# Performance work log

Measured on AMD Instinct MI355X. Metric: run time of the kernel, lower is better.

## Reference

```python
import jax, jax.numpy as jnp
import numpy as np

B, S, H = 2, 2048, 2048
E, I, SH = 8, 768, 5632
TOP_K = 2


def setup_inputs() -> dict:
    key = jax.random.key(0)
    ks = jax.random.split(key, 8)
    sc = lambda *shape: 1.0 / np.sqrt(shape[-2] if len(shape) > 1 else 1.0)
    return {
        "hidden_states": jax.random.normal(ks[0], (B, S, H), jnp.float32),
        "router_w": jax.random.normal(ks[1], (H, E), jnp.float32) * (1.0 / np.sqrt(H)),
        "expert_gate_up_w": jax.random.normal(ks[2], (E, H, 2 * I), jnp.float32) * (1.0 / np.sqrt(H)),
        "expert_down_w": jax.random.normal(ks[3], (E, I, H), jnp.float32) * (1.0 / np.sqrt(I)),
        "shared_gate_w": jax.random.normal(ks[4], (H, SH), jnp.float32) * (1.0 / np.sqrt(H)),
        "shared_up_w": jax.random.normal(ks[5], (H, SH), jnp.float32) * (1.0 / np.sqrt(H)),
        "shared_down_w": jax.random.normal(ks[6], (SH, H), jnp.float32) * (1.0 / np.sqrt(SH)),
        "shared_expert_gate_w": jax.random.normal(ks[7], (H, 1), jnp.float32) * (1.0 / np.sqrt(H)),
    }


def reference(hidden_states, router_w, expert_gate_up_w, expert_down_w,
              shared_gate_w, shared_up_w, shared_down_w, shared_expert_gate_w):
    b, s, h = hidden_states.shape
    x = hidden_states.reshape(-1, h)  # [T, H]

    # Shared expert (SwiGLU) gated by sigmoid scalar gate per token.
    gate = jax.nn.silu((x @ shared_gate_w).astype(jnp.float32)).astype(x.dtype)
    shared_out = (gate * (x @ shared_up_w)) @ shared_down_w  # [T, H]
    shared_out = jax.nn.sigmoid(x @ shared_expert_gate_w) * shared_out

    # Router: softmax -> top-k -> renormalize -> dense routing weights [E, T].
    router_logits = x @ router_w  # [T, E]
    router_probs = jax.nn.softmax(router_logits, axis=-1)
    top_p, top_i = jax.lax.top_k(router_probs, TOP_K)  # [T, k]
    top_p = top_p / jnp.sum(top_p, axis=-1, keepdims=True)
    one_hot = jax.nn.one_hot(top_i, E, dtype=top_p.dtype)  # [T, k, E]
    routing_full = jnp.sum(one_hot * top_p[..., None], axis=1)  # [T, E]
    routing_full = routing_full.T.astype(x.dtype)  # [E, T]

    # Dense per-expert SwiGLU over all tokens (as in source einsums).
    gate_up = jnp.einsum('th,ehm->etm', x, expert_gate_up_w)  # [E, T, 2I]
    g, u = jnp.split(gate_up, 2, axis=-1)
    g = jax.nn.silu(g.astype(jnp.float32)).astype(x.dtype)
    expert_out = jnp.einsum('eti,eih->eth', u * g, expert_down_w)  # [E, T, H]

    expert_contribution = jnp.sum(expert_out * routing_full[:, :, None], axis=0)  # [T, H]
    out = (expert_contribution + shared_out).reshape(b, s, h)
    return out, router_logits
```

## Files before the change

### kernel.cpp

```cpp
#include <hip/hip_runtime.h>
#include <hip/hip_bf16.h>
#include <stdint.h>

#define DEVFN static __device__ __forceinline__

typedef __attribute__((ext_vector_type(8))) short bf16x8;
typedef __attribute__((ext_vector_type(4))) float f32x4;
typedef unsigned short u16;
typedef unsigned int u32;
typedef unsigned long long u64;

DEVFN u16 f2bf(float f) {
    union { float f; u32 u; } v; v.f = f;
    u32 r = v.u + 0x7FFFu + ((v.u >> 16) & 1u);
    return (u16)(r >> 16);
}

DEVFN void g2l16(const void* g, void* l) {
    __builtin_amdgcn_global_load_lds(
        (const __attribute__((address_space(1))) u32*)g,
        (__attribute__((address_space(3))) u32*)l, 16, 0, 0);
}

DEVFN void hbar() {
    __asm__ __volatile__("" ::: "memory");
    __builtin_amdgcn_s_barrier();
    __asm__ __volatile__("" ::: "memory");
}
DEVFN void vm4() { asm volatile("s_waitcnt vmcnt(4)" ::: "memory"); }
DEVFN void vm0() { asm volatile("s_waitcnt vmcnt(0)" ::: "memory"); }

#define MFMA16(a, b, c) __builtin_amdgcn_mfma_f32_16x16x32_bf16(a, b, c, 0, 0, 0)

__global__ __launch_bounds__(512, 2) void gemm8_swiglu_k(
    const u16* __restrict__ A, const u16* __restrict__ Bg,
    const u16* __restrict__ Bu, u16* __restrict__ out,
    int K, int nx, int ldc)
{
    extern __shared__ char smraw[];
    char* smA = smraw;
    char* smB = smraw + 65536;

    const int tid = threadIdx.x;
    const int lane = tid & 63, wv = tid >> 6;
    const int wm = wv >> 2, wn = wv & 3;
    const int l15 = lane & 15, kg = lane >> 4;

    const int nwg = gridDim.x;
    const int id = (blockIdx.x & 7) * (nwg >> 3) + (blockIdx.x >> 3);
    const int m0 = (id / nx) * 256, n0 = (id % nx) * 128;

    const u16* Ap  = A  + (long)m0 * K;
    const u16* Bgp = Bg + (long)n0 * K;
    const u16* Bup = Bu + (long)n0 * K;

    f32x4 accg[8][2], accu[8][2];
#pragma unroll
    for (int i = 0; i < 8; ++i)
#pragma unroll
        for (int j = 0; j < 2; ++j) {
            accg[i][j] = f32x4{0.f, 0.f, 0.f, 0.f};
            accu[i][j] = f32x4{0.f, 0.f, 0.f, 0.f};
        }

    auto stA = [&](int kt, int hh, int buf) {
        const u16* src = Ap + ((long)hh * 128) * K + kt * 64;
        char* dst = smA + buf * 32768 + hh * 16384;
#pragma unroll
        for (int i = 0; i < 2; ++i) {
            int slot = i * 512 + tid;
            int row = slot >> 3, ch = slot & 7;
            g2l16(src + (long)row * K + ((ch ^ (row & 7)) << 3), dst + slot * 16);
        }
    };
    auto stB = [&](int kt, int hh, int buf) {
        const u16* src = (hh ? Bup : Bgp) + kt * 64;
        char* dst = smB + buf * 32768 + hh * 16384;
#pragma unroll
        for (int i = 0; i < 2; ++i) {
            int slot = i * 512 + tid;
            int row = slot >> 3, ch = slot & 7;
            g2l16(src + (long)row * K + ((ch ^ (row & 7)) << 3), dst + slot * 16);
        }
    };
    auto frag = [&](const char* base, int r, int c) -> bf16x8 {
        return *(const __attribute__((address_space(3))) bf16x8*)
            (base + r * 128 + (((c) ^ (r & 7)) << 4));
    };

    stA(0, 0, 0); stA(0, 1, 0);
    stB(0, 0, 0); stB(0, 1, 0);
    stB(1, 0, 1); stB(1, 1, 1);
    vm4();
    hbar();

    const int nk = K >> 6;
    for (int kt = 0; kt < nk; kt += 2) {
        const bool more = (kt + 2) < nk;
#pragma unroll
        for (int h = 0; h < 2; ++h) {
            const char* ab = smA + h * 32768;
            const char* bb = smB + h * 32768;
            bf16x8 bgv[2][2], buv[2][2];
#pragma unroll
            for (int p = 0; p < 4; ++p) {
                if (p == 0) {
#pragma unroll
                    for (int fn = 0; fn < 2; ++fn)
#pragma unroll
                        for (int s = 0; s < 2; ++s) {
                            int rB = wn * 32 + fn * 16 + l15;
                            bgv[fn][s] = frag(bb, rB, s * 4 + kg);
                            buv[fn][s] = frag(bb + 16384, rB, s * 4 + kg);
                        }
                }
                bf16x8 av[2][2];
#pragma unroll
                for (int am = 0; am < 2; ++am)
#pragma unroll
                    for (int s = 0; s < 2; ++s)
                        av[am][s] = frag(ab, wm * 128 + (p * 2 + am) * 16 + l15,
                                         s * 4 + kg);
                if (h == 0) {
                    if (p == 0)      { stA(kt + 1, 0, 1); stA(kt + 1, 1, 1); }
                    else if (p == 1) { if (more) stB(kt + 2, 0, 0); }
                    else if (p == 2) { if (more) stB(kt + 2, 1, 0); }
                    else             { if (more) vm4(); else vm0(); }
                } else {
                    if (more) {
                        if (p == 0)      stA(kt + 2, 0, 0);
                        else if (p == 1) stA(kt + 2, 1, 0);
                        else if (p == 2) stB(kt + 3, 0, 1);
                        else             { stB(kt + 3, 1, 1); vm4(); }
                    }
                }
                hbar();
                __builtin_amdgcn_sched_barrier(0);
                __builtin_amdgcn_s_setprio(1);
#pragma unroll
                for (int am = 0; am < 2; ++am)
#pragma unroll
                    for (int s = 0; s < 2; ++s)
#pragma unroll
                        for (int fn = 0; fn < 2; ++fn) {
                            accg[p * 2 + am][fn] = MFMA16(av[am][s], bgv[fn][s],
                                                          accg[p * 2 + am][fn]);
                            accu[p * 2 + am][fn] = MFMA16(av[am][s], buv[fn][s],
                                                          accu[p * 2 + am][fn]);
                        }
                __builtin_amdgcn_s_setprio(0);
                __builtin_amdgcn_sched_barrier(0);
                hbar();
            }
        }
    }

    const int lq = lane >> 4;
#pragma unroll
    for (int fm = 0; fm < 8; ++fm)
#pragma unroll
        for (int j = 0; j < 4; ++j) {
            int row = m0 + wm * 128 + fm * 16 + lq * 4 + j;
#pragma unroll
            for (int fn = 0; fn < 2; ++fn) {
                int col = n0 + wn * 32 + fn * 16 + l15;
                float g = accg[fm][fn][j], u = accu[fm][fn][j];
                float s = g * (1.f / (1.f + __expf(-g))) * u;
                out[(long)row * ldc + col] = f2bf(s);
            }
        }
}

__global__ __launch_bounds__(512, 2) void gemm8e_swiglu_k(
    const u16* __restrict__ xb, const u16* __restrict__ Beg,
    const u16* __restrict__ Beu, const int* __restrict__ tok,
    const int* __restrict__ cntp, u16* __restrict__ eact,
    int K, int ldc, int cap)
{
    const int e = blockIdx.z;
    const int m0 = blockIdx.y * 256;
    if (m0 >= cntp[e]) return;
    const int n0 = blockIdx.x * 128;

    extern __shared__ char smraw[];
    char* smA = smraw;
    char* smB = smraw + 65536;

    const int tid = threadIdx.x;
    const int lane = tid & 63, wv = tid >> 6;
    const int wm = wv >> 2, wn = wv & 3;
    const int l15 = lane & 15, kg = lane >> 4;

    const int r0 = tid >> 3, ch = tid & 7;
    const int swz = (ch ^ (r0 & 7)) << 3;
    const int* tseg = tok + (long)e * cap + m0;
    const u16* pa00 = xb + (long)tseg[r0] * K + swz;
    const u16* pa01 = xb + (long)tseg[64 + r0] * K + swz;
    const u16* pa10 = xb + (long)tseg[128 + r0] * K + swz;
    const u16* pa11 = xb + (long)tseg[192 + r0] * K + swz;

    const u16* Bgp = Beg + ((long)e * ldc + n0) * K;
    const u16* Bup = Beu + ((long)e * ldc + n0) * K;

    f32x4 accg[8][2], accu[8][2];
#pragma unroll
    for (int i = 0; i < 8; ++i)
#pragma unroll
        for (int j = 0; j < 2; ++j) {
            accg[i][j] = f32x4{0.f, 0.f, 0.f, 0.f};
            accu[i][j] = f32x4{0.f, 0.f, 0.f, 0.f};
        }

    auto stA = [&](int kt, int hh, int buf) {
        char* dst = smA + buf * 32768 + hh * 16384;
        const u16* p0 = hh ? pa10 : pa00;
        const u16* p1 = hh ? pa11 : pa01;
        g2l16(p0 + kt * 64, dst + (long)tid * 16);
        g2l16(p1 + kt * 64, dst + (long)(512 + tid) * 16);
    };
    auto stB = [&](int kt, int hh, int buf) {
        const u16* src = (hh ? Bup : Bgp) + kt * 64;
        char* dst = smB + buf * 32768 + hh * 16384;
#pragma unroll
        for (int i = 0; i < 2; ++i) {
            int slot = i * 512 + tid;
            int row = slot >> 3, c = slot & 7;
            g2l16(src + (long)row * K + ((c ^ (row & 7)) << 3), dst + slot * 16);
        }
    };
    auto frag = [&](const char* base, int r, int c) -> bf16x8 {
        return *(const __attribute__((address_space(3))) bf16x8*)
            (base + r * 128 + (((c) ^ (r & 7)) << 4));
    };

    stA(0, 0, 0); stA(0, 1, 0);
    stB(0, 0, 0); stB(0, 1, 0);
    stB(1, 0, 1); stB(1, 1, 1);
    vm4();
    hbar();

    const int nk = K >> 6;
    for (int kt = 0; kt < nk; kt += 2) {
        const bool more = (kt + 2) < nk;
#pragma unroll
        for (int h = 0; h < 2; ++h) {
            const char* ab = smA + h * 32768;
            const char* bb = smB + h * 32768;
            bf16x8 bgv[2][2], buv[2][2];
#pragma unroll
            for (int p = 0; p < 4; ++p) {
                if (p == 0) {
#pragma unroll
                    for (int fn = 0; fn < 2; ++fn)
#pragma unroll
                        for (int s = 0; s < 2; ++s) {
                            int rB = wn * 32 + fn * 16 + l15;
                            bgv[fn][s] = frag(bb, rB, s * 4 + kg);
                            buv[fn][s] = frag(bb + 16384, rB, s * 4 + kg);
                        }
                }
                bf16x8 av[2][2];
#pragma unroll
                for (int am = 0; am < 2; ++am)
#pragma unroll
                    for (int s = 0; s < 2; ++s)
                        av[am][s] = frag(ab, wm * 128 + (p * 2 + am) * 16 + l15,
                                         s * 4 + kg);
                if (h == 0) {
                    if (p == 0)      { stA(kt + 1, 0, 1); stA(kt + 1, 1, 1); }
                    else if (p == 1) { if (more) stB(kt + 2, 0, 0); }
                    else if (p == 2) { if (more) stB(kt + 2, 1, 0); }
                    else             { if (more) vm4(); else vm0(); }
                } else {
                    if (more) {
                        if (p == 0)      stA(kt + 2, 0, 0);
                        else if (p == 1) stA(kt + 2, 1, 0);
                        else if (p == 2) stB(kt + 3, 0, 1);
                        else             { stB(kt + 3, 1, 1); vm4(); }
                    }
                }
                hbar();
                __builtin_amdgcn_sched_barrier(0);
                __builtin_amdgcn_s_setprio(1);
#pragma unroll
                for (int am = 0; am < 2; ++am)
#pragma unroll
                    for (int s = 0; s < 2; ++s)
#pragma unroll
                        for (int fn = 0; fn < 2; ++fn) {
                            accg[p * 2 + am][fn] = MFMA16(av[am][s], bgv[fn][s],
                                                          accg[p * 2 + am][fn]);
                            accu[p * 2 + am][fn] = MFMA16(av[am][s], buv[fn][s],
                                                          accu[p * 2 + am][fn]);
                        }
                __builtin_amdgcn_s_setprio(0);
                __builtin_amdgcn_sched_barrier(0);
                hbar();
            }
        }
    }

    const int lq = lane >> 4;
#pragma unroll
    for (int fm = 0; fm < 8; ++fm)
#pragma unroll
        for (int j = 0; j < 4; ++j) {
            long row = (long)e * cap + m0 + wm * 128 + fm * 16 + lq * 4 + j;
#pragma unroll
            for (int fn = 0; fn < 2; ++fn) {
                int col = n0 + wn * 32 + fn * 16 + l15;
                float g = accg[fm][fn][j], u = accu[fm][fn][j];
                float s = g * (1.f / (1.f + __expf(-g))) * u;
                eact[row * ldc + col] = f2bf(s);
            }
        }
}

__global__ __launch_bounds__(512, 2) void gemm8_downks_k(
    const u16* __restrict__ A, const u16* __restrict__ B,
    float* __restrict__ out, const float* __restrict__ sig,
    int K, int nkh, int ldc)
{
    extern __shared__ char smraw[];
    char* smA = smraw;
    char* smB = smraw + 65536;

    const int tid = threadIdx.x;
    const int lane = tid & 63, wv = tid >> 6;
    const int wm = wv >> 2, wn = wv & 3;
    const int l15 = lane & 15, kg = lane >> 4;

    const int m0 = blockIdx.y * 256, n0 = blockIdx.x * 256;
    const long k0 = (long)blockIdx.z * nkh * 64;

    const u16* Ap  = A + (long)m0 * K + k0;
    const u16* Blo = B + (long)n0 * K + k0;
    const u16* Bhi = B + (long)(n0 + 128) * K + k0;

    f32x4 accg[8][2], accu[8][2];
#pragma unroll
    for (int i = 0; i < 8; ++i)
#pragma unroll
        for (int j = 0; j < 2; ++j) {
            accg[i][j] = f32x4{0.f, 0.f, 0.f, 0.f};
            accu[i][j] = f32x4{0.f, 0.f, 0.f, 0.f};
        }

    auto stA = [&](int kt, int hh, int buf) {
        const u16* src = Ap + ((long)hh * 128) * K + kt * 64;
        char* dst = smA + buf * 32768 + hh * 16384;
#pragma unroll
        for (int i = 0; i < 2; ++i) {
            int slot = i * 512 + tid;
            int row = slot >> 3, ch = slot & 7;
            g2l16(src + (long)row * K + ((ch ^ (row & 7)) << 3), dst + slot * 16);
        }
    };
    auto stB = [&](int kt, int hh, int buf) {
        const u16* src = (hh ? Bhi : Blo) + kt * 64;
        char* dst = smB + buf * 32768 + hh * 16384;
#pragma unroll
        for (int i = 0; i < 2; ++i) {
            int slot = i * 512 + tid;
            int row = slot >> 3, ch = slot & 7;
            g2l16(src + (long)row * K + ((ch ^ (row & 7)) << 3), dst + slot * 16);
        }
    };
    auto frag = [&](const char* base, int r, int c) -> bf16x8 {
        return *(const __attribute__((address_space(3))) bf16x8*)
            (base + r * 128 + (((c) ^ (r & 7)) << 4));
    };

    stA(0, 0, 0); stA(0, 1, 0);
    stB(0, 0, 0); stB(0, 1, 0);
    stB(1, 0, 1); stB(1, 1, 1);
    vm4();
    hbar();

    const int nk = nkh;
    for (int kt = 0; kt < nk; kt += 2) {
        const bool more = (kt + 2) < nk;
#pragma unroll
        for (int h = 0; h < 2; ++h) {
            const char* ab = smA + h * 32768;
            const char* bb = smB + h * 32768;
            bf16x8 bgv[2][2], buv[2][2];
#pragma unroll
            for (int p = 0; p < 4; ++p) {
                if (p == 0) {
#pragma unroll
                    for (int fn = 0; fn < 2; ++fn)
#pragma unroll
                        for (int s = 0; s < 2; ++s) {
                            int rB = wn * 32 + fn * 16 + l15;
                            bgv[fn][s] = frag(bb, rB, s * 4 + kg);
                            buv[fn][s] = frag(bb + 16384, rB, s * 4 + kg);
                        }
                }
                bf16x8 av[2][2];
#pragma unroll
                for (int am = 0; am < 2; ++am)
#pragma unroll
                    for (int s = 0; s < 2; ++s)
                        av[am][s] = frag(ab, wm * 128 + (p * 2 + am) * 16 + l15,
                                         s * 4 + kg);
                if (h == 0) {
                    if (p == 0)      { stA(kt + 1, 0, 1); stA(kt + 1, 1, 1); }
                    else if (p == 1) { if (more) stB(kt + 2, 0, 0); }
                    else if (p == 2) { if (more) stB(kt + 2, 1, 0); }
                    else             { if (more) vm4(); else vm0(); }
                } else {
                    if (more) {
                        if (p == 0)      stA(kt + 2, 0, 0);
                        else if (p == 1) stA(kt + 2, 1, 0);
                        else if (p == 2) stB(kt + 3, 0, 1);
                        else             { stB(kt + 3, 1, 1); vm4(); }
                    }
                }
                hbar();
                __builtin_amdgcn_sched_barrier(0);
                __builtin_amdgcn_s_setprio(1);
#pragma unroll
                for (int am = 0; am < 2; ++am)
#pragma unroll
                    for (int s = 0; s < 2; ++s)
#pragma unroll
                        for (int fn = 0; fn < 2; ++fn) {
                            accg[p * 2 + am][fn] = MFMA16(av[am][s], bgv[fn][s],
                                                          accg[p * 2 + am][fn]);
                            accu[p * 2 + am][fn] = MFMA16(av[am][s], buv[fn][s],
                                                          accu[p * 2 + am][fn]);
                        }
                __builtin_amdgcn_s_setprio(0);
                __builtin_amdgcn_sched_barrier(0);
                hbar();
            }
        }
    }

    const int lq = lane >> 4;
#pragma unroll
    for (int fm = 0; fm < 8; ++fm)
#pragma unroll
        for (int j = 0; j < 4; ++j) {
            int row = m0 + wm * 128 + fm * 16 + lq * 4 + j;
            float s = sig[row];
#pragma unroll
            for (int fn = 0; fn < 2; ++fn) {
                int col = n0 + wn * 32 + fn * 16 + l15;
                atomicAdd(out + (long)row * ldc + col, accg[fm][fn][j] * s);
                atomicAdd(out + (long)row * ldc + col + 128, accu[fm][fn][j] * s);
            }
        }
}

template<int NSLOT>
DEVFN void stage(const u16* __restrict__ src, int ldk, u16* lds, int tid) {
#pragma unroll
    for (int i = 0; i < NSLOT / 256; ++i) {
        int slot = i * 256 + tid;
        int row = slot >> 2, chunk = slot & 3;
        int kg = chunk ^ ((row >> 1) & 3);
        g2l16(src + (long)row * ldk + kg * 8, lds + slot * 8);
    }
}

DEVFN bf16x8 ld_frag(const u16* lds, int row, int kg) {
    int chunk = kg ^ ((row >> 1) & 3);
    const u16* p = lds + row * 32 + chunk * 8;
    return *(const __attribute__((address_space(3))) bf16x8*)p;
}

__global__ __launch_bounds__(256) void gemm_down_moe_k(
    const u16* __restrict__ eact, const u16* __restrict__ Bed,
    float* __restrict__ out, const int* __restrict__ tok,
    const float* __restrict__ wrow, const int* __restrict__ cntp,
    int K, int ldc, int cap)
{
    const int e = blockIdx.z;
    const int m0 = blockIdx.y * 128;
    if (m0 >= cntp[e]) return;
    const int n0 = blockIdx.x * 128;

    __shared__ u16 sm[2][8192];
    const int tid = threadIdx.x;
    const int lane = tid & 63, wv = tid >> 6;
    const int wm = wv >> 1, wn = wv & 1;
    const u16* Ab = eact + ((long)e * cap + m0) * K;
    const u16* Bb = Bed + (long)e * ldc * K + (long)n0 * K;

    f32x4 acc[4][4];
#pragma unroll
    for (int i = 0; i < 4; ++i)
#pragma unroll
        for (int j = 0; j < 4; ++j) acc[i][j] = f32x4{0.f, 0.f, 0.f, 0.f};

    stage<512>(Ab, K, &sm[0][0], tid);
    stage<512>(Bb, K, &sm[0][4096], tid);

    const int nk = K >> 5;
    for (int kt = 0; kt < nk; ++kt) {
        const int cur = kt & 1;
        __syncthreads();
        if (kt + 1 < nk) {
            stage<512>(Ab + (kt + 1) * 32, K, &sm[cur ^ 1][0], tid);
            stage<512>(Bb + (kt + 1) * 32, K, &sm[cur ^ 1][4096], tid);
        }
        const int l15 = lane & 15, kg = lane >> 4;
        bf16x8 av[4], bv[4];
#pragma unroll
        for (int f = 0; f < 4; ++f) {
            av[f] = ld_frag(&sm[cur][0],    wm * 64 + f * 16 + l15, kg);
            bv[f] = ld_frag(&sm[cur][4096], wn * 64 + f * 16 + l15, kg);
        }
#pragma unroll
        for (int fm = 0; fm < 4; ++fm)
#pragma unroll
            for (int fn = 0; fn < 4; ++fn)
                acc[fm][fn] = MFMA16(av[fm], bv[fn], acc[fm][fn]);
    }

    const int l15 = lane & 15, lq = lane >> 4;
#pragma unroll
    for (int fm = 0; fm < 4; ++fm) {
#pragma unroll
        for (int j = 0; j < 4; ++j) {
            long crow = (long)e * cap + m0 + wm * 64 + fm * 16 + lq * 4 + j;
            float w = wrow[crow];
            if (w != 0.f) {
                long t = tok[crow];
#pragma unroll
                for (int fn = 0; fn < 4; ++fn) {
                    int col = n0 + wn * 64 + fn * 16 + l15;
                    atomicAdd(out + t * ldc + col, acc[fm][fn][j] * w);
                }
            }
        }
    }
}

__global__ __launch_bounds__(256) void router_k(
    const float* __restrict__ x, const float* __restrict__ rw,
    const float* __restrict__ sgw, float* __restrict__ logits,
    int2* __restrict__ te, float2* __restrict__ tw,
    float* __restrict__ sig, int T, int H)
{
    const int tid = threadIdx.x, lane = tid & 63, wv = tid >> 6;
    const int t = blockIdx.x * 4 + wv;
    const float* xr = x + (long)t * H;
    float acc[8] = {0, 0, 0, 0, 0, 0, 0, 0};
    float as = 0.f;
    for (int h = lane; h < H; h += 64) {
        float xv = xr[h];
        const float* r = rw + h * 8;
#pragma unroll
        for (int e = 0; e < 8; ++e) acc[e] += xv * r[e];
        as += xv * sgw[h];
    }
#pragma unroll
    for (int off = 32; off; off >>= 1) {
#pragma unroll
        for (int e = 0; e < 8; ++e) acc[e] += __shfl_xor(acc[e], off);
        as += __shfl_xor(as, off);
    }
    if (lane == 0) {
        float mx = acc[0];
#pragma unroll
        for (int e = 1; e < 8; ++e) mx = fmaxf(mx, acc[e]);
        float p[8], sum = 0.f;
#pragma unroll
        for (int e = 0; e < 8; ++e) { p[e] = expf(acc[e] - mx); sum += p[e]; }
        int i1 = 0;
#pragma unroll
        for (int e = 1; e < 8; ++e) if (p[e] > p[i1]) i1 = e;
        int i2 = (i1 == 0) ? 1 : 0;
#pragma unroll
        for (int e = 0; e < 8; ++e) if (e != i1 && p[e] > p[i2]) i2 = e;
        float den = p[i1] + p[i2];
        te[t] = make_int2(i1, i2);
        tw[t] = make_float2(p[i1] / den, p[i2] / den);
#pragma unroll
        for (int e = 0; e < 8; ++e) logits[(long)t * 8 + e] = acc[e];
        sig[t] = 1.f / (1.f + expf(-as));
    }
}

__global__ __launch_bounds__(256) void compact_k(
    const int2* __restrict__ te, const float2* __restrict__ tw,
    int* __restrict__ tok, float* __restrict__ wrow,
    int* __restrict__ cntp, int T, int cap)
{
    const int e = blockIdx.x;
    const int tid = threadIdx.x, lane = tid & 63, wv = tid >> 6;
    __shared__ int wtot[4];
    int cnt = 0;
    for (int c0 = 0; c0 < T; c0 += 256) {
        int t = c0 + tid;
        int2 ids = te[t];
        float2 ws = tw[t];
        float w = (ids.x == e) ? ws.x : ((ids.y == e) ? ws.y : -1.f);
        bool sel = (w >= 0.f);
        u64 b = __ballot(sel);
        int rln = __popcll(b & ((1ull << lane) - 1ull));
        if (lane == 0) wtot[wv] = __popcll(b);
        __syncthreads();
        int rank = rln, tot = 0;
#pragma unroll
        for (int k = 0; k < 4; ++k) { if (k < wv) rank += wtot[k]; tot += wtot[k]; }
        if (sel) {
            int pos = cnt + rank;
            if (pos < cap) {
                tok[(long)e * cap + pos] = t;
                wrow[(long)e * cap + pos] = w;
            }
        }
        cnt += tot;
        __syncthreads();
    }
    if (cnt > cap) cnt = cap;
    int cp = (cnt + 255) & ~255;
    if (cp > cap) cp = cap;
    for (int p = cnt + tid; p < cp; p += 256) {
        tok[(long)e * cap + p] = 0;
        wrow[(long)e * cap + p] = 0.f;
    }
    if (tid == 0) cntp[e] = cp;
}

__global__ __launch_bounds__(256) void transpose_k(
    const float* __restrict__ src0, long src_zstr, int src_ld,
    u16* __restrict__ dst0, long dst_zstr, int dst_ld)
{
    __shared__ float tile[32][33];
    const float* src = src0 + (long)blockIdx.z * src_zstr;
    u16* dst = dst0 + (long)blockIdx.z * dst_zstr;
    int r0 = blockIdx.y * 32, c0 = blockIdx.x * 32;
    int tx = threadIdx.x, ty = threadIdx.y;
#pragma unroll
    for (int k = 0; k < 4; ++k)
        tile[ty + 8 * k][tx] = src[(long)(r0 + ty + 8 * k) * src_ld + c0 + tx];
    __syncthreads();
#pragma unroll
    for (int k = 0; k < 4; ++k)
        dst[(long)(c0 + ty + 8 * k) * dst_ld + r0 + tx] = f2bf(tile[tx][ty + 8 * k]);
}

__global__ __launch_bounds__(256) void cvt_x_k(const float* __restrict__ x,
                                               u16* __restrict__ xb)
{
    long i = ((long)blockIdx.x * 256 + threadIdx.x) * 4;
    float4 v = *(const float4*)(x + i);
    union { u16 s[4]; uint2 v2; } o;
    o.s[0] = f2bf(v.x); o.s[1] = f2bf(v.y); o.s[2] = f2bf(v.z); o.s[3] = f2bf(v.w);
    *(uint2*)(xb + i) = o.v2;
}

extern "C" void kernel_launch(void* const* d_in, const int* in_sizes, int n_in,
                              void* d_out, int out_size, void* d_ws, size_t ws_size,
                              hipStream_t stream) {
    (void)in_sizes; (void)n_in; (void)out_size; (void)ws_size;
    const int Hd = 2048, E = 8, I = 768, SH = 5632, T = 4096, CAP = 2048;

    const float* x    = (const float*)d_in[0];
    const float* rw   = (const float*)d_in[1];
    const float* egu  = (const float*)d_in[2];
    const float* edw  = (const float*)d_in[3];
    const float* sgw  = (const float*)d_in[4];
    const float* suw  = (const float*)d_in[5];
    const float* sdw  = (const float*)d_in[6];
    const float* segw = (const float*)d_in[7];
    float* out = (float*)d_out;
    float* logits = out + (size_t)T * Hd;

    char* wsp = (char*)d_ws;
    size_t off = 0;
    auto alloc = [&](size_t bytes) {
        void* p = wsp + off; off += (bytes + 255) & ~(size_t)255; return p;
    };
    u16* xb   = (u16*)alloc((size_t)T * Hd * 2);
    u16* Bgs  = (u16*)alloc((size_t)SH * Hd * 2);
    u16* Bus  = (u16*)alloc((size_t)SH * Hd * 2);
    u16* Bds  = (u16*)alloc((size_t)Hd * SH * 2);
    u16* Beg  = (u16*)alloc((size_t)E * I * Hd * 2);
    u16* Beu  = (u16*)alloc((size_t)E * I * Hd * 2);
    u16* Bed  = (u16*)alloc((size_t)E * Hd * I * 2);
    u16* hs   = (u16*)alloc((size_t)T * SH * 2);
    u16* eact = (u16*)alloc((size_t)E * CAP * I * 2);
    int2*   te   = (int2*)alloc((size_t)T * 8);
    float2* tw   = (float2*)alloc((size_t)T * 8);
    int*    tok  = (int*)alloc((size_t)E * CAP * 4);
    float*  wrow = (float*)alloc((size_t)E * CAP * 4);
    int*    cntp = (int*)alloc(64);
    float*  sig  = (float*)alloc((size_t)T * 4);

    hipFuncSetAttribute((const void*)gemm8_swiglu_k,
                        hipFuncAttributeMaxDynamicSharedMemorySize, 131072);
    hipFuncSetAttribute((const void*)gemm8e_swiglu_k,
                        hipFuncAttributeMaxDynamicSharedMemorySize, 131072);
    hipFuncSetAttribute((const void*)gemm8_downks_k,
                        hipFuncAttributeMaxDynamicSharedMemorySize, 131072);

    dim3 tb(32, 8);
    hipMemsetAsync(out, 0, (size_t)T * Hd * 4, stream);
    cvt_x_k<<<(T * Hd) / 1024, 256, 0, stream>>>(x, xb);
    router_k<<<T / 4, 256, 0, stream>>>(x, rw, segw, logits, te, tw, sig, T, Hd);
    compact_k<<<E, 256, 0, stream>>>(te, tw, tok, wrow, cntp, T, CAP);

    transpose_k<<<dim3(SH / 32, Hd / 32), tb, 0, stream>>>(sgw, 0, SH, Bgs, 0, Hd);
    transpose_k<<<dim3(SH / 32, Hd / 32), tb, 0, stream>>>(suw, 0, SH, Bus, 0, Hd);
    transpose_k<<<dim3(Hd / 32, SH / 32), tb, 0, stream>>>(sdw, 0, Hd, Bds, 0, SH);
    transpose_k<<<dim3(I / 32, Hd / 32, E), tb, 0, stream>>>(
        egu, (long)Hd * 2 * I, 2 * I, Beg, (long)I * Hd, Hd);
    transpose_k<<<dim3(I / 32, Hd / 32, E), tb, 0, stream>>>(
        egu + I, (long)Hd * 2 * I, 2 * I, Beu, (long)I * Hd, Hd);
    transpose_k<<<dim3(Hd / 32, I / 32, E), tb, 0, stream>>>(
        edw, (long)I * Hd, Hd, Bed, (long)Hd * I, I);

    gemm8_swiglu_k<<<dim3((SH / 128) * (T / 256)), 512, 131072, stream>>>(
        xb, Bgs, Bus, hs, Hd, SH / 128, SH);
    gemm8_downks_k<<<dim3(Hd / 256, T / 256, 2), 512, 131072, stream>>>(
        hs, Bds, out, sig, SH, (SH / 64) / 2, Hd);
    gemm8e_swiglu_k<<<dim3(I / 128, CAP / 256, E), 512, 131072, stream>>>(
        xb, Beg, Beu, tok, cntp, eact, Hd, I, CAP);
    gemm_down_moe_k<<<dim3(Hd / 128, CAP / 128, E), 256, 0, stream>>>(
        eact, Bed, out, tok, wrow, cntp, I, Hd, CAP);
}
```

Measured before the change: 603.2 us.

## Rework down-projection GEMMs: drop split-K atomics, 256x128 tiles, larger transposes

The shared-expert down GEMM no longer splits K across two blocks with atomic adds. It now uses 256x128 tiles over the full K, stores results directly (which removes the output memset) and remaps block ids in an XCD-aware order. The routed-expert down GEMM moves from a 128x128 tile, 256-thread kernel to the same 512-thread, 256x128, double-buffered LDS pipeline used by the other GEMMs. The weight transpose kernel now uses 64x64 tiles. This cuts atomic traffic and the memset and raises per-block reuse, in exchange for fewer blocks in flight per GEMM and an ordering dependency, since the expert kernel's atomics must run after the shared kernel's plain stores.

```diff
diff --git a/kernel.cpp b/kernel.cpp
--- a/kernel.cpp
+++ b/kernel.cpp
@@ -28,6 +28,7 @@
     __asm__ __volatile__("" ::: "memory");
 }
 DEVFN void vm4() { asm volatile("s_waitcnt vmcnt(4)" ::: "memory"); }
+DEVFN void vm2() { asm volatile("s_waitcnt vmcnt(2)" ::: "memory"); }
 DEVFN void vm0() { asm volatile("s_waitcnt vmcnt(0)" ::: "memory"); }
 
 #define MFMA16(a, b, c) __builtin_amdgcn_mfma_f32_16x16x32_bf16(a, b, c, 0, 0, 0)
@@ -316,10 +317,10 @@
         }
 }
 
-__global__ __launch_bounds__(512, 2) void gemm8_downks_k(
+__global__ __launch_bounds__(512, 2) void gemm8_down_k(
     const u16* __restrict__ A, const u16* __restrict__ B,
-    float* __restrict__ out, const float* __restrict__ sig,
-    int K, int nkh, int ldc)
+    float* __restrict__ C, const float* __restrict__ gvec,
+    int K, int nx, int ldc)
 {
     extern __shared__ char smraw[];
     char* smA = smraw;
@@ -330,21 +331,18 @@
     const int wm = wv >> 2, wn = wv & 3;
     const int l15 = lane & 15, kg = lane >> 4;
 
-    const int m0 = blockIdx.y * 256, n0 = blockIdx.x * 256;
-    const long k0 = (long)blockIdx.z * nkh * 64;
-
-    const u16* Ap  = A + (long)m0 * K + k0;
-    const u16* Blo = B + (long)n0 * K + k0;
-    const u16* Bhi = B + (long)(n0 + 128) * K + k0;
-
-    f32x4 accg[8][2], accu[8][2];
+    const int nwg = gridDim.x;
+    const int id = (blockIdx.x & 7) * (nwg >> 3) + (blockIdx.x >> 3);
+    const int m0 = (id / nx) * 256, n0 = (id % nx) * 128;
+
+    const u16* Ap = A + (long)m0 * K;
+    const u16* Bp = B + (long)n0 * K;
+
+    f32x4 acc[8][2];
 #pragma unroll
     for (int i = 0; i < 8; ++i)
 #pragma unroll
-        for (int j = 0; j < 2; ++j) {
-            accg[i][j] = f32x4{0.f, 0.f, 0.f, 0.f};
-            accu[i][j] = f32x4{0.f, 0.f, 0.f, 0.f};
-        }
+        for (int j = 0; j < 2; ++j) acc[i][j] = f32x4{0.f, 0.f, 0.f, 0.f};
 
     auto stA = [&](int kt, int hh, int buf) {
         const u16* src = Ap + ((long)hh * 128) * K + kt * 64;
@@ -356,9 +354,9 @@
             g2l16(src + (long)row * K + ((ch ^ (row & 7)) << 3), dst + slot * 16);
         }
     };
-    auto stB = [&](int kt, int hh, int buf) {
-        const u16* src = (hh ? Bhi : Blo) + kt * 64;
-        char* dst = smB + buf * 32768 + hh * 16384;
+    auto stB1 = [&](int kt, int buf) {
+        const u16* src = Bp + kt * 64;
+        char* dst = smB + buf * 16384;
 #pragma unroll
         for (int i = 0; i < 2; ++i) {
             int slot = i * 512 + tid;
@@ -372,65 +370,57 @@
     };
 
     stA(0, 0, 0); stA(0, 1, 0);
-    stB(0, 0, 0); stB(0, 1, 0);
-    stB(1, 0, 1); stB(1, 1, 1);
-    vm4();
+    stB1(0, 0);
+    stB1(1, 1);
+    vm2();
     hbar();
 
-    const int nk = nkh;
+    const int nk = K >> 6;
     for (int kt = 0; kt < nk; kt += 2) {
         const bool more = (kt + 2) < nk;
 #pragma unroll
         for (int h = 0; h < 2; ++h) {
             const char* ab = smA + h * 32768;
-            const char* bb = smB + h * 32768;
-            bf16x8 bgv[2][2], buv[2][2];
-#pragma unroll
-            for (int p = 0; p < 4; ++p) {
+            const char* bb = smB + h * 16384;
+            bf16x8 bv[2][2];
+#pragma unroll
+            for (int p = 0; p < 2; ++p) {
                 if (p == 0) {
 #pragma unroll
                     for (int fn = 0; fn < 2; ++fn)
 #pragma unroll
-                        for (int s = 0; s < 2; ++s) {
-                            int rB = wn * 32 + fn * 16 + l15;
-                            bgv[fn][s] = frag(bb, rB, s * 4 + kg);
-                            buv[fn][s] = frag(bb + 16384, rB, s * 4 + kg);
-                        }
-                }
-                bf16x8 av[2][2];
-#pragma unroll
-                for (int am = 0; am < 2; ++am)
+                        for (int s = 0; s < 2; ++s)
+                            bv[fn][s] = frag(bb, wn * 32 + fn * 16 + l15,
+                                             s * 4 + kg);
+                }
+                bf16x8 av[4][2];
+#pragma unroll
+                for (int am = 0; am < 4; ++am)
 #pragma unroll
                     for (int s = 0; s < 2; ++s)
-                        av[am][s] = frag(ab, wm * 128 + (p * 2 + am) * 16 + l15,
+                        av[am][s] = frag(ab, wm * 128 + (p * 4 + am) * 16 + l15,
                                          s * 4 + kg);
                 if (h == 0) {
                     if (p == 0)      { stA(kt + 1, 0, 1); stA(kt + 1, 1, 1); }
-                    else if (p == 1) { if (more) stB(kt + 2, 0, 0); }
-                    else if (p == 2) { if (more) stB(kt + 2, 1, 0); }
-                    else             { if (more) vm4(); else vm0(); }
+                    else             { if (more) { stB1(kt + 2, 0); vm2(); }
+                                       else vm0(); }
                 } else {
                     if (more) {
-                        if (p == 0)      stA(kt + 2, 0, 0);
-                        else if (p == 1) stA(kt + 2, 1, 0);
-                        else if (p == 2) stB(kt + 3, 0, 1);
-                        else             { stB(kt + 3, 1, 1); vm4(); }
+                        if (p == 0)  { stA(kt + 2, 0, 0); stA(kt + 2, 1, 0); }
+                        else         { stB1(kt + 3, 1); vm2(); }
                     }
                 }
                 hbar();
                 __builtin_amdgcn_sched_barrier(0);
                 __builtin_amdgcn_s_setprio(1);
 #pragma unroll
-                for (int am = 0; am < 2; ++am)
+                for (int am = 0; am < 4; ++am)
 #pragma unroll
                     for (int s = 0; s < 2; ++s)
 #pragma unroll
-                        for (int fn = 0; fn < 2; ++fn) {
-                            accg[p * 2 + am][fn] = MFMA16(av[am][s], bgv[fn][s],
-                                                          accg[p * 2 + am][fn]);
-                            accu[p * 2 + am][fn] = MFMA16(av[am][s], buv[fn][s],
-                                                          accu[p * 2 + am][fn]);
-                        }
+                        for (int fn = 0; fn < 2; ++fn)
+                            acc[p * 4 + am][fn] = MFMA16(av[am][s], bv[fn][s],
+                                                         acc[p * 4 + am][fn]);
                 __builtin_amdgcn_s_setprio(0);
                 __builtin_amdgcn_sched_barrier(0);
                 hbar();
@@ -444,99 +434,144 @@
 #pragma unroll
         for (int j = 0; j < 4; ++j) {
             int row = m0 + wm * 128 + fm * 16 + lq * 4 + j;
-            float s = sig[row];
+            float gmul = gvec[row];
 #pragma unroll
             for (int fn = 0; fn < 2; ++fn) {
                 int col = n0 + wn * 32 + fn * 16 + l15;
-                atomicAdd(out + (long)row * ldc + col, accg[fm][fn][j] * s);
-                atomicAdd(out + (long)row * ldc + col + 128, accu[fm][fn][j] * s);
-            }
-        }
-}
-
-template<int NSLOT>
-DEVFN void stage(const u16* __restrict__ src, int ldk, u16* lds, int tid) {
-#pragma unroll
-    for (int i = 0; i < NSLOT / 256; ++i) {
-        int slot = i * 256 + tid;
-        int row = slot >> 2, chunk = slot & 3;
-        int kg = chunk ^ ((row >> 1) & 3);
-        g2l16(src + (long)row * ldk + kg * 8, lds + slot * 8);
-    }
-}
-
-DEVFN bf16x8 ld_frag(const u16* lds, int row, int kg) {
-    int chunk = kg ^ ((row >> 1) & 3);
-    const u16* p = lds + row * 32 + chunk * 8;
-    return *(const __attribute__((address_space(3))) bf16x8*)p;
-}
-
-__global__ __launch_bounds__(256) void gemm_down_moe_k(
+                C[(long)row * ldc + col] = acc[fm][fn][j] * gmul;
+            }
+        }
+}
+
+__global__ __launch_bounds__(512, 2) void gemm8_edown_k(
     const u16* __restrict__ eact, const u16* __restrict__ Bed,
     float* __restrict__ out, const int* __restrict__ tok,
     const float* __restrict__ wrow, const int* __restrict__ cntp,
-    int K, int ldc, int cap)
+    int K, int Hd, int cap)
 {
     const int e = blockIdx.z;
-    const int m0 = blockIdx.y * 128;
+    const int m0 = blockIdx.y * 256;
     if (m0 >= cntp[e]) return;
     const int n0 = blockIdx.x * 128;
 
-    __shared__ u16 sm[2][8192];
+    extern __shared__ char smraw[];
+    char* smA = smraw;
+    char* smB = smraw + 65536;
+
     const int tid = threadIdx.x;
     const int lane = tid & 63, wv = tid >> 6;
-    const int wm = wv >> 1, wn = wv & 1;
-    const u16* Ab = eact + ((long)e * cap + m0) * K;
-    const u16* Bb = Bed + (long)e * ldc * K + (long)n0 * K;
-
-    f32x4 acc[4][4];
-#pragma unroll
-    for (int i = 0; i < 4; ++i)
-#pragma unroll
-        for (int j = 0; j < 4; ++j) acc[i][j] = f32x4{0.f, 0.f, 0.f, 0.f};
-
-    stage<512>(Ab, K, &sm[0][0], tid);
-    stage<512>(Bb, K, &sm[0][4096], tid);
-
-    const int nk = K >> 5;
-    for (int kt = 0; kt < nk; ++kt) {
-        const int cur = kt & 1;
-        __syncthreads();
-        if (kt + 1 < nk) {
-            stage<512>(Ab + (kt + 1) * 32, K, &sm[cur ^ 1][0], tid);
-            stage<512>(Bb + (kt + 1) * 32, K, &sm[cur ^ 1][4096], tid);
-        }
-        const int l15 = lane & 15, kg = lane >> 4;
-        bf16x8 av[4], bv[4];
-#pragma unroll
-        for (int f = 0; f < 4; ++f) {
-            av[f] = ld_frag(&sm[cur][0],    wm * 64 + f * 16 + l15, kg);
-            bv[f] = ld_frag(&sm[cur][4096], wn * 64 + f * 16 + l15, kg);
-        }
-#pragma unroll
-        for (int fm = 0; fm < 4; ++fm)
-#pragma unroll
-            for (int fn = 0; fn < 4; ++fn)
-                acc[fm][fn] = MFMA16(av[fm], bv[fn], acc[fm][fn]);
-    }
-
-    const int l15 = lane & 15, lq = lane >> 4;
-#pragma unroll
-    for (int fm = 0; fm < 4; ++fm) {
+    const int wm = wv >> 2, wn = wv & 3;
+    const int l15 = lane & 15, kg = lane >> 4;
+
+    const u16* Ap = eact + ((long)e * cap + m0) * K;
+    const u16* Bp = Bed + ((long)e * Hd + n0) * K;
+
+    f32x4 acc[8][2];
+#pragma unroll
+    for (int i = 0; i < 8; ++i)
+#pragma unroll
+        for (int j = 0; j < 2; ++j) acc[i][j] = f32x4{0.f, 0.f, 0.f, 0.f};
+
+    auto stA = [&](int kt, int hh, int buf) {
+        const u16* src = Ap + ((long)hh * 128) * K + kt * 64;
+        char* dst = smA + buf * 32768 + hh * 16384;
+#pragma unroll
+        for (int i = 0; i < 2; ++i) {
+            int slot = i * 512 + tid;
+            int row = slot >> 3, ch = slot & 7;
+            g2l16(src + (long)row * K + ((ch ^ (row & 7)) << 3), dst + slot * 16);
+        }
+    };
+    auto stB1 = [&](int kt, int buf) {
+        const u16* src = Bp + kt * 64;
+        char* dst = smB + buf * 16384;
+#pragma unroll
+        for (int i = 0; i < 2; ++i) {
+            int slot = i * 512 + tid;
+            int row = slot >> 3, ch = slot & 7;
+            g2l16(src + (long)row * K + ((ch ^ (row & 7)) << 3), dst + slot * 16);
+        }
+    };
+    auto frag = [&](const char* base, int r, int c) -> bf16x8 {
+        return *(const __attribute__((address_space(3))) bf16x8*)
+            (base + r * 128 + (((c) ^ (r & 7)) << 4));
+    };
+
+    stA(0, 0, 0); stA(0, 1, 0);
+    stB1(0, 0);
+    stB1(1, 1);
+    vm2();
+    hbar();
+
+    const int nk = K >> 6;
+    for (int kt = 0; kt < nk; kt += 2) {
+        const bool more = (kt + 2) < nk;
+#pragma unroll
+        for (int h = 0; h < 2; ++h) {
+            const char* ab = smA + h * 32768;
+            const char* bb = smB + h * 16384;
+            bf16x8 bv[2][2];
+#pragma unroll
+            for (int p = 0; p < 2; ++p) {
+                if (p == 0) {
+#pragma unroll
+                    for (int fn = 0; fn < 2; ++fn)
+#pragma unroll
+                        for (int s = 0; s < 2; ++s)
+                            bv[fn][s] = frag(bb, wn * 32 + fn * 16 + l15,
+                                             s * 4 + kg);
+                }
+                bf16x8 av[4][2];
+#pragma unroll
+                for (int am = 0; am < 4; ++am)
+#pragma unroll
+                    for (int s = 0; s < 2; ++s)
+                        av[am][s] = frag(ab, wm * 128 + (p * 4 + am) * 16 + l15,
+                                         s * 4 + kg);
+                if (h == 0) {
+                    if (p == 0)      { stA(kt + 1, 0, 1); stA(kt + 1, 1, 1); }
+                    else             { if (more) { stB1(kt + 2, 0); vm2(); }
+                                       else vm0(); }
+                } else {
+                    if (more) {
+                        if (p == 0)  { stA(kt + 2, 0, 0); stA(kt + 2, 1, 0); }
+                        else         { stB1(kt + 3, 1); vm2(); }
+                    }
+                }
+                hbar();
+                __builtin_amdgcn_sched_barrier(0);
+                __builtin_amdgcn_s_setprio(1);
+#pragma unroll
+                for (int am = 0; am < 4; ++am)
+#pragma unroll
+                    for (int s = 0; s < 2; ++s)
+#pragma unroll
+                        for (int fn = 0; fn < 2; ++fn)
+                            acc[p * 4 + am][fn] = MFMA16(av[am][s], bv[fn][s],
+                                                         acc[p * 4 + am][fn]);
+                __builtin_amdgcn_s_setprio(0);
+                __builtin_amdgcn_sched_barrier(0);
+                hbar();
+            }
+        }
+    }
+
+    const int lq = lane >> 4;
+#pragma unroll
+    for (int fm = 0; fm < 8; ++fm)
 #pragma unroll
         for (int j = 0; j < 4; ++j) {
-            long crow = (long)e * cap + m0 + wm * 64 + fm * 16 + lq * 4 + j;
+            long crow = (long)e * cap + m0 + wm * 128 + fm * 16 + lq * 4 + j;
             float w = wrow[crow];
             if (w != 0.f) {
                 long t = tok[crow];
 #pragma unroll
-                for (int fn = 0; fn < 4; ++fn) {
-                    int col = n0 + wn * 64 + fn * 16 + l15;
-                    atomicAdd(out + t * ldc + col, acc[fm][fn][j] * w);
-                }
-            }
-        }
-    }
+                for (int fn = 0; fn < 2; ++fn) {
+                    int col = n0 + wn * 32 + fn * 16 + l15;
+                    atomicAdd(out + t * Hd + col, acc[fm][fn][j] * w);
+                }
+            }
+        }
 }
 
 __global__ __launch_bounds__(256) void router_k(
@@ -631,18 +666,18 @@
     const float* __restrict__ src0, long src_zstr, int src_ld,
     u16* __restrict__ dst0, long dst_zstr, int dst_ld)
 {
-    __shared__ float tile[32][33];
+    __shared__ float tile[64][65];
     const float* src = src0 + (long)blockIdx.z * src_zstr;
     u16* dst = dst0 + (long)blockIdx.z * dst_zstr;
-    int r0 = blockIdx.y * 32, c0 = blockIdx.x * 32;
-    int tx = threadIdx.x, ty = threadIdx.y;
-#pragma unroll
-    for (int k = 0; k < 4; ++k)
-        tile[ty + 8 * k][tx] = src[(long)(r0 + ty + 8 * k) * src_ld + c0 + tx];
+    int r0 = blockIdx.y * 64, c0 = blockIdx.x * 64;
+    int tx = threadIdx.x & 63, ty = threadIdx.x >> 6;
+#pragma unroll
+    for (int k = 0; k < 16; ++k)
+        tile[ty + 4 * k][tx] = src[(long)(r0 + ty + 4 * k) * src_ld + c0 + tx];
     __syncthreads();
 #pragma unroll
-    for (int k = 0; k < 4; ++k)
-        dst[(long)(c0 + ty + 8 * k) * dst_ld + r0 + tx] = f2bf(tile[tx][ty + 8 * k]);
+    for (int k = 0; k < 16; ++k)
+        dst[(long)(c0 + ty + 4 * k) * dst_ld + r0 + tx] = f2bf(tile[tx][ty + 4 * k]);
 }
 
 __global__ __launch_bounds__(256) void cvt_x_k(const float* __restrict__ x,
@@ -697,31 +732,31 @@
                         hipFuncAttributeMaxDynamicSharedMemorySize, 131072);
     hipFuncSetAttribute((const void*)gemm8e_swiglu_k,
                         hipFuncAttributeMaxDynamicSharedMemorySize, 131072);
-    hipFuncSetAttribute((const void*)gemm8_downks_k,
-                        hipFuncAttributeMaxDynamicSharedMemorySize, 131072);
-
-    dim3 tb(32, 8);
-    hipMemsetAsync(out, 0, (size_t)T * Hd * 4, stream);
+    hipFuncSetAttribute((const void*)gemm8_down_k,
+                        hipFuncAttributeMaxDynamicSharedMemorySize, 98304);
+    hipFuncSetAttribute((const void*)gemm8_edown_k,
+                        hipFuncAttributeMaxDynamicSharedMemorySize, 98304);
+
     cvt_x_k<<<(T * Hd) / 1024, 256, 0, stream>>>(x, xb);
     router_k<<<T / 4, 256, 0, stream>>>(x, rw, segw, logits, te, tw, sig, T, Hd);
     compact_k<<<E, 256, 0, stream>>>(te, tw, tok, wrow, cntp, T, CAP);
 
-    transpose_k<<<dim3(SH / 32, Hd / 32), tb, 0, stream>>>(sgw, 0, SH, Bgs, 0, Hd);
-    transpose_k<<<dim3(SH / 32, Hd / 32), tb, 0, stream>>>(suw, 0, SH, Bus, 0, Hd);
-    transpose_k<<<dim3(Hd / 32, SH / 32), tb, 0, stream>>>(sdw, 0, Hd, Bds, 0, SH);
-    transpose_k<<<dim3(I / 32, Hd / 32, E), tb, 0, stream>>>(
+    transpose_k<<<dim3(SH / 64, Hd / 64), 256, 0, stream>>>(sgw, 0, SH, Bgs, 0, Hd);
+    transpose_k<<<dim3(SH / 64, Hd / 64), 256, 0, stream>>>(suw, 0, SH, Bus, 0, Hd);
+    transpose_k<<<dim3(Hd / 64, SH / 64), 256, 0, stream>>>(sdw, 0, Hd, Bds, 0, SH);
+    transpose_k<<<dim3(I / 64, Hd / 64, E), 256, 0, stream>>>(
         egu, (long)Hd * 2 * I, 2 * I, Beg, (long)I * Hd, Hd);
-    transpose_k<<<dim3(I / 32, Hd / 32, E), tb, 0, stream>>>(
+    transpose_k<<<dim3(I / 64, Hd / 64, E), 256, 0, stream>>>(
         egu + I, (long)Hd * 2 * I, 2 * I, Beu, (long)I * Hd, Hd);
-    transpose_k<<<dim3(Hd / 32, I / 32, E), tb, 0, stream>>>(
+    transpose_k<<<dim3(Hd / 64, I / 64, E), 256, 0, stream>>>(
         edw, (long)I * Hd, Hd, Bed, (long)Hd * I, I);
 
     gemm8_swiglu_k<<<dim3((SH / 128) * (T / 256)), 512, 131072, stream>>>(
         xb, Bgs, Bus, hs, Hd, SH / 128, SH);
-    gemm8_downks_k<<<dim3(Hd / 256, T / 256, 2), 512, 131072, stream>>>(
-        hs, Bds, out, sig, SH, (SH / 64) / 2, Hd);
+    gemm8_down_k<<<dim3((Hd / 128) * (T / 256)), 512, 98304, stream>>>(
+        hs, Bds, out, sig, SH, Hd / 128, Hd);
     gemm8e_swiglu_k<<<dim3(I / 128, CAP / 256, E), 512, 131072, stream>>>(
         xb, Beg, Beu, tok, cntp, eact, Hd, I, CAP);
-    gemm_down_moe_k<<<dim3(Hd / 128, CAP / 128, E), 256, 0, stream>>>(
+    gemm8_edown_k<<<dim3(Hd / 128, CAP / 256, E), 512, 98304, stream>>>(
         eact, Bed, out, tok, wrow, cntp, I, Hd, CAP);
 }
```

Measured after the change: 580.4 us. 3.8% less time.
